# Optimization experiments

Measured on AMD Instinct MI355X. Metric: run time of the kernel, lower is better.

Reference implementation:

```python
import jax, jax.numpy as jnp
from jax import lax
import numpy as np

BS, T, DA, DZ, K = 64, 512, 16, 32, 3


def _lstm_layer(x, Wih, Whh, bih, bhh):
    # x: [B, T, in], PyTorch LSTM gate order i,f,g,o; zero initial state
    B = x.shape[0]
    H = Whh.shape[1]
    b = bih + bhh

    def step(carry, xt):
        h, c = carry
        g = xt @ Wih.T + h @ Whh.T + b  # [B, 4H]
        i, f, gg, o = jnp.split(g, 4, axis=-1)
        c = jax.nn.sigmoid(f) * c + jax.nn.sigmoid(i) * jnp.tanh(gg)
        h = jax.nn.sigmoid(o) * jnp.tanh(c)
        return (h, c), h

    h0 = jnp.zeros((B, H), x.dtype)
    _, hs = lax.scan(step, (h0, h0), jnp.swapaxes(x, 0, 1))
    return jnp.swapaxes(hs, 0, 1)


def setup_inputs() -> dict:
    key = jax.random.key(0)
    ks = jax.random.split(key, 12)
    a = jax.random.normal(ks[0], (BS, T, DA), jnp.float32)
    # mixture dynamics / emission matrices, kept near identity for stability
    A = 0.95 * jnp.eye(DZ, dtype=jnp.float32) + 0.02 * jax.random.normal(ks[1], (K, T, DZ, DZ), jnp.float32)
    C = jnp.eye(DA, DZ, dtype=jnp.float32) + 0.05 * jax.random.normal(ks[2], (K, T, DA, DZ), jnp.float32)
    R = 0.1 * jnp.eye(DA, dtype=jnp.float32)
    Q = 0.1 * jnp.eye(DZ, dtype=jnp.float32)
    mu0 = jnp.zeros((DZ,), jnp.float32)
    sigma0 = jnp.eye(DZ, dtype=jnp.float32)
    H4 = 4 * K  # LSTM hidden size = K
    Wih0 = 0.1 * jax.random.normal(ks[3], (H4, DA), jnp.float32)
    Whh0 = 0.1 * jax.random.normal(ks[4], (H4, K), jnp.float32)
    bih0 = 0.1 * jax.random.normal(ks[5], (H4,), jnp.float32)
    bhh0 = 0.1 * jax.random.normal(ks[6], (H4,), jnp.float32)
    Wih1 = 0.1 * jax.random.normal(ks[7], (H4, K), jnp.float32)
    Whh1 = 0.1 * jax.random.normal(ks[8], (H4, K), jnp.float32)
    bih1 = 0.1 * jax.random.normal(ks[9], (H4,), jnp.float32)
    bhh1 = 0.1 * jax.random.normal(ks[10], (H4,), jnp.float32)
    return {"a": a, "A": A, "C": C, "R": R, "Q": Q, "mu0": mu0, "sigma0": sigma0,
            "Wih0": Wih0, "Whh0": Whh0, "bih0": bih0, "bhh0": bhh0,
            "Wih1": Wih1, "Whh1": Whh1, "bih1": bih1, "bhh1": bhh1}


def reference(a, A, C, R, Q, mu0, sigma0, Wih0, Whh0, bih0, bhh0, Wih1, Whh1, bih1, bhh1):
    bs, T, da = a.shape
    dz = A.shape[-1]
    # dynamics network: 2-layer LSTM + softmax mixture weights alpha [bs,T,K]
    h = _lstm_layer(a, Wih0, Whh0, bih0, bhh0)
    h = _lstm_layer(h, Wih1, Whh1, bih1, bhh1)
    alpha = jax.nn.softmax(h, axis=-1)
    # mix per-mode matrices; time-major [T,bs,.,.]
    At = jnp.einsum('btk,ktij->tbij', alpha, A)
    Ct = jnp.einsum('btk,ktij->tbij', alpha, C)
    a_tm = jnp.swapaxes(a, 0, 1)  # [T,bs,da]
    I = jnp.eye(dz, dtype=a.dtype)
    mu_f0 = jnp.broadcast_to(mu0, (bs, dz))
    sig_f0 = jnp.broadcast_to(sigma0, (bs, dz, dz))

    def fstep(carry, inp):
        mu_f, mu_p, sig_p = carry  # prev filtered mean, predicted mean/cov
        a_t, A_t, C_t = inp
        # NOTE: residual uses previous *filtered* mean, matching the source code
        r = a_t - jnp.einsum('bij,bj->bi', C_t, mu_f)
        Ct_T = jnp.swapaxes(C_t, -1, -2)
        S = C_t @ sig_p @ Ct_T + R
        Kg = sig_p @ Ct_T @ jnp.linalg.inv(S)
        mu_new = mu_p + jnp.einsum('bij,bj->bi', Kg, r)
        sig_new = (I - Kg @ C_t) @ sig_p
        mu_p_new = jnp.einsum('bij,bj->bi', A_t, mu_new)
        sig_p_new = A_t @ sig_new @ jnp.swapaxes(A_t, -1, -2) + Q
        return (mu_new, mu_p_new, sig_p_new), (mu_new, sig_new, mu_p_new, sig_p_new)

    _, (mu_f, sig_f, mu_p, sig_p) = lax.scan(
        fstep, (mu_f0, mu_f0, sig_f0), (a_tm, At, Ct))

    # RTS smoothing (backward recursion), faithful to smooth()
    def sstep(carry, inp):
        mu_n, sig_n = carry
        mu_ft, sig_ft, mu_pt, sig_pt, A_next = inp
        J = sig_ft @ jnp.swapaxes(A_next, -1, -2) @ jnp.linalg.inv(sig_pt)
        mu_s = mu_ft + jnp.einsum('bij,bj->bi', J, mu_n - mu_pt)
        sig_s = sig_ft + J @ (sig_n - sig_pt)
        return (mu_s, sig_s), (mu_s, sig_s)

    _, (mu_s_rest, sig_s_rest) = lax.scan(
        sstep, (mu_f[-1], sig_f[-1]),
        (mu_f[:-1], sig_f[:-1], mu_p[:-1], sig_p[:-1], At[1:]),
        reverse=True)
    mu_s = jnp.concatenate([mu_s_rest, mu_f[-1:]], axis=0)   # [T,bs,dz]
    sig_s = jnp.concatenate([sig_s_rest, sig_f[-1:]], axis=0)  # [T,bs,dz,dz]
    out = jnp.concatenate([mu_s, sig_s.reshape(T, bs, dz * dz)], axis=-1)
    return jnp.swapaxes(out, 0, 1)  # [bs, T, dz + dz*dz]
```

## Files before the change

kernel.cpp:

```cpp
#include <hip/hip_runtime.h>
#include <hip/hip_bf16.h>

#define BSZ 64
#define TT  512
#define DA  16
#define DZ  32
#define NG  12
#define NT  256

typedef __hip_bfloat16 bf;

#define FP32_R0 0x3DCCCCCDu

__device__ __forceinline__ int mode_(const void* Rm){
  return (((const unsigned*)Rm)[0] == FP32_R0) ? 0 : 1;
}
__device__ __forceinline__ float LD(const void* p, size_t i, int b16){
  return b16 ? __bfloat162float(((const bf*)p)[i]) : ((const float*)p)[i];
}
__device__ __forceinline__ void STO(void* p, size_t i, float v, int b16){
  if (b16) ((bf*)p)[i] = __float2bfloat16(v);
  else     ((float*)p)[i] = v;
}
__device__ __forceinline__ float osan_(double vd, float code){
// ... 27 lines not shown
    for (int g=0;g<NG;++g){
      #pragma unroll
      for (int j=0;j<3;++j){ w0[g][j]=LD(Whh0,(size_t)g*3+j,b16); wi1[g][j]=LD(Wih1,(size_t)g*3+j,b16); w1[g][j]=LD(Whh1,(size_t)g*3+j,b16); }
      bb[g] = LD(bih1,g,b16) + LD(bhh1,g,b16);
    }
    float h1[3]={0,0,0}, c1[3]={0,0,0}, h2[3]={0,0,0}, c2[3]={0,0,0};
    for (int t=0;t<TT;++t){
      const float* xr = sxw + t*NG;
      float g1[NG];
      #pragma unroll
      for (int g=0;g<NG;++g) g1[g] = xr[g] + w0[g][0]*h1[0]+w0[g][1]*h1[1]+w0[g][2]*h1[2];
      #pragma unroll
      for (int j=0;j<3;++j){
        float iv=sigm_(g1[j]), fv=sigm_(g1[3+j]), gv=tanh_(g1[6+j]), ov=sigm_(g1[9+j]);
        c1[j] = fv*c1[j] + iv*gv;
        h1[j] = ov*tanh_(c1[j]);
      }
      float g2[NG];
      #pragma unroll
      for (int g=0;g<NG;++g) g2[g] = bb[g] + wi1[g][0]*h1[0]+wi1[g][1]*h1[1]+wi1[g][2]*h1[2]
                                            + w1[g][0]*h2[0]+w1[g][1]*h2[1]+w1[g][2]*h2[2];
      #pragma unroll
      for (int j=0;j<3;++j){
        float iv=sigm_(g2[j]), fv=sigm_(g2[3+j]), gv=tanh_(g2[6+j]), ov=sigm_(g2[9+j]);
        c2[j] = fv*c2[j] + iv*gv;
        h2[j] = ov*tanh_(c2[j]);
      }
      float m = fmaxf(h2[0], fmaxf(h2[1], h2[2]));
      float e0=__expf(h2[0]-m), e1=__expf(h2[1]-m), e2=__expf(h2[2]-m);
      float inv = 1.0f/(e0+e1+e2);
      salp[t*3+0]=e0*inv; salp[t*3+1]=e1*inv; salp[t*3+2]=e2*inv;
    }
  }
  __syncthreads();
}

__global__ __launch_bounds__(256) void k_alpha(
  const void* __restrict__ a, const void* __restrict__ Rm,
  const void* __restrict__ Wih0, const void* __restrict__ Whh0,
  const void* __restrict__ bih0, const void* __restrict__ bhh0,
  const void* __restrict__ Wih1, const void* __restrict__ Whh1,
  const void* __restrict__ bih1, const void* __restrict__ bhh1,
  float* __restrict__ alws)
{
  const int b16 = mode_(Rm);
  const int b = blockIdx.x, tid = threadIdx.x;
  __shared__ float sxw[TT*NG];
  __shared__ float salp[TT*3];
  alpha_stage_(b, tid, NT, b16, a, Wih0, bih0, bhh0, Whh0, Wih1, Whh1, bih1, bhh1,
               sxw, salp);
  for (int e=tid;e<TT*3;e+=NT) alws[(size_t)b*TT*3+e] = salp[e];
}

__global__ __launch_bounds__(256) void k_fwd(
  const void* __restrict__ a, const void* __restrict__ Am,
  const void* __restrict__ Cm, const void* __restrict__ Rm,
  const void* __restrict__ Qm, const void* __restrict__ mu0,
  const void* __restrict__ sig0,
  const void* __restrict__ Wih0, const void* __restrict__ Whh0,
  const void* __restrict__ bih0, const void* __restrict__ bhh0,
  const void* __restrict__ Wih1, const void* __restrict__ Whh1,
  const void* __restrict__ bih1, const void* __restrict__ bhh1,
  const float* __restrict__ alws,
  void* __restrict__ out)
{
  const int b16 = mode_(Rm);
  const int b = blockIdx.x, tid = threadIdx.x;
  __shared__ double dpool[4240];
  __shared__ float sAt[1056], sCt[528], sQ[1056], sR[272], sPCt[544], sKg[544];
  __shared__ float salp[TT*3];
  __shared__ double dMu[32], dMup[32], dr[16];
  double* dPp  = dpool;
  double* dAP  = dpool+1056;
  double* dKCP = dpool+2112;
  double* dCP  = dpool+3168;
  double* dAugS= dpool+3696;
  double* dMinv= dpool+3968;

  if (alws){
    for (int e=tid;e<TT*3;e+=NT) salp[e] = alws[(size_t)b*TT*3+e];
    __syncthreads();
  } else {
    alpha_stage_(b, tid, NT, b16, a, Wih0, bih0, bhh0, Whh0, Wih1, Whh1, bih1, bhh1,
                 (float*)dpool, salp);
  }

  for (int e=tid;e<1024;e+=NT){ int i=e>>5,j=e&31;
    sQ[i*33+j]  = LD(Qm,e,b16);
    dPp[i*33+j] = (double)LD(sig0,e,b16); }
  for (int e=tid;e<256;e+=NT){ int i=e>>4,j=e&15; sR[i*17+j] = LD(Rm,e,b16); }
  if (tid<32){ double m = (double)LD(mu0,tid,b16); dMu[tid]=m; dMup[tid]=m; }
  __syncthreads();

  const int i0 = tid>>5, j0 = tid&31;
  const int i4 = tid>>4, j4 = tid&15;

  float pA0[4],pA1[4],pA2[4],pC0[2],pC1[2],pC2[2];
  {
    size_t o0=0, o1=(size_t)TT*1024, o2=(size_t)2*TT*1024;
    #pragma unroll
    for (int q=0;q<4;++q){ int e=tid+q*NT; pA0[q]=LD(Am,o0+e,b16); pA1[q]=LD(Am,o1+e,b16); pA2[q]=LD(Am,o2+e,b16); }
    size_t c0=0, c1=(size_t)TT*512, c2=(size_t)2*TT*512;
    #pragma unroll
    for (int q=0;q<2;++q){ int e=tid+q*NT; pC0[q]=LD(Cm,c0+e,b16); pC1[q]=LD(Cm,c1+e,b16); pC2[q]=LD(Cm,c2+e,b16); }
  }

  for (int t=0;t<TT;++t){
    const size_t ob = ((size_t)b*TT+t)*1056;
    {
      float a0=salp[t*3+0], a1=salp[t*3+1], a2=salp[t*3+2];
      #pragma unroll
      for (int q=0;q<4;++q){ int e=tid+q*NT; int i=e>>5,j=e&31;
        sAt[i*33+j] = a0*pA0[q]+a1*pA1[q]+a2*pA2[q]; }
      #pragma unroll
      for (int q=0;q<2;++q){ int e=tid+q*NT; int i=e>>5,j=e&31;
        sCt[i*33+j] = a0*pC0[q]+a1*pC1[q]+a2*pC2[q]; }
    }
    if (t+1<TT){
      size_t o0=(size_t)(t+1)*1024, o1=(size_t)(TT+t+1)*1024, o2=(size_t)(2*TT+t+1)*1024;
      #pragma unroll
      for (int q=0;q<4;++q){ int e=tid+q*NT; pA0[q]=LD(Am,o0+e,b16); pA1[q]=LD(Am,o1+e,b16); pA2[q]=LD(Am,o2+e,b16); }
      size_t c0=(size_t)(t+1)*512, c1=(size_t)(TT+t+1)*512, c2=(size_t)(2*TT+t+1)*512;
      #pragma unroll
      for (int q=0;q<2;++q){ int e=tid+q*NT; pC0[q]=LD(Cm,c0+e,b16); pC1[q]=LD(Cm,c1+e,b16); pC2[q]=LD(Cm,c2+e,b16); }
    }
    __syncthreads();

    {
      double col[32];
      #pragma unroll
      for (int k=0;k<32;++k) col[k] = dPp[k*33+j0];
      double A0=0.0, A1=0.0;
      #pragma unroll
      for (int k=0;k<32;++k){
        A0 += (double)sCt[i0*33+k]*col[k];
        A1 += (double)sCt[(i0+8)*33+k]*col[k]; }
      dCP[i0*33+j0]=A0; dCP[(i0+8)*33+j0]=A1;
      double B0=0.0, B1v=0.0;
      #pragma unroll
      for (int m=0;m<32;++m){ double cv=(double)sCt[j4*33+m];
        B0  += dPp[i4*33+m]*cv;
        B1v += dPp[(i4+16)*33+m]*cv; }
      sPCt[i4*17+j4]=(float)B0; sPCt[(i4+16)*17+j4]=(float)B1v;
    }
    if (tid<16){ double s = (double)LD(a,((size_t)b*TT+t)*DA+tid,b16);
      #pragma unroll
      for (int k=0;k<32;++k) s -= (double)sCt[tid*33+k]*dMu[k];
      dr[tid]=s; }
    __syncthreads();

    if (tid < 64){
      #pragma unroll
      for (int u=0;u<4;++u){ int e=(tid<<2)+u; int i=e>>4, j=e&15;
        double v=(double)sR[i*17+j];
        #pragma unroll
        for (int k=0;k<32;++k) v += dCP[i*33+k]*(double)sCt[j*33+k];
        dAugS[i*17+j]=v; }
      const int r = tid>>2, q = tid&3, cbase = q*8;
      double Rg[8];
      #pragma unroll
      for (int u=0;u<8;++u){
        int c = cbase+u;
        Rg[u] = (c<16) ? dAugS[r*17+c] : ((c-16)==r ? 1.0 : 0.0);
      }
      #pragma unroll
      for (int kp=0;kp<16;++kp){
        double pv = __shfl(Rg[kp&7], (kp<<2)|(kp>>3), 64);
        if (!(fabs(pv)>1e-300)) pv=1.0;
        double ip = 1.0/pv;
        if (r==kp){
          #pragma unroll
          for (int u=0;u<8;++u){ int c=cbase+u; if (c>kp) Rg[u]*=ip; }
        }
        double rf = __shfl(Rg[kp&7], (tid&0x3C)|(kp>>3), 64);
        #pragma unroll
        for (int u=0;u<8;++u){
          double pr = __shfl(Rg[u], (kp<<2)|q, 64);
          int c=cbase+u;
          if (r!=kp && c>kp) Rg[u] -= rf*pr;
        }
      }
      if (q>=2){
        #pragma unroll
        for (int u=0;u<8;++u){ int k=cbase+u-16; dMinv[r*17+k]=Rg[u]; }
      }
    } else {
      for (int e=tid-64; e<1024; e+=192){ int i=e>>5,j=e&31; double acc=0.0;
        #pragma unroll
        for (int k=0;k<32;++k) acc += (double)sAt[i*33+k]*dPp[k*33+j];
        dAP[i*33+j]=acc; }
    }
    __syncthreads();

    {
      double col[16];
      #pragma unroll
      for (int l=0;l<16;++l) col[l] = dMinv[l*17+j4];
      double A0=0.0, A1=0.0;
      #pragma unroll
      for (int l=0;l<16;++l){
        A0 += (double)sPCt[i4*17+l]*col[l];
        A1 += (double)sPCt[(i4+16)*17+l]*col[l]; }
      sKg[i4*17+j4]=(float)A0; sKg[(i4+16)*17+j4]=(float)A1;
    }
    __syncthreads();

    {
      double col[16];
      #pragma unroll
      for (int l=0;l<16;++l) col[l] = dCP[l*33+j0];
      double A0=0.0,A1=0.0,A2=0.0,A3=0.0;
      #pragma unroll
      for (int l=0;l<16;++l){
        A0 += (double)sKg[i0*17+l]*col[l];
        A1 += (double)sKg[(i0+8)*17+l]*col[l];
        A2 += (double)sKg[(i0+16)*17+l]*col[l];
        A3 += (double)sKg[(i0+24)*17+l]*col[l]; }
      dKCP[i0*33+j0]=A0; dKCP[(i0+8)*33+j0]=A1;
      dKCP[(i0+16)*33+j0]=A2; dKCP[(i0+24)*33+j0]=A3;
    }
    if (tid<32){ double s=dMup[tid];
      #pragma unroll
      for (int k=0;k<16;++k) s += (double)sKg[tid*17+k]*dr[k];
      dMu[tid]=s;
      STO(out, ob+tid, osan_(s,5300.0f), b16); }
    __syncthreads();

    {
      double colK[32];
      #pragma unroll
      for (int k=0;k<32;++k) colK[k] = dKCP[k*33+j0];
      double pf0 = dPp[i0*33+j0]      - colK[0*0+ (0)];
      (void)pf0;
      double P0 = dPp[i0*33+j0]      - dKCP[i0*33+j0];
      double P1 = dPp[(i0+8)*33+j0]  - dKCP[(i0+8)*33+j0];
      double P2 = dPp[(i0+16)*33+j0] - dKCP[(i0+16)*33+j0];
      double P3 = dPp[(i0+24)*33+j0] - dKCP[(i0+24)*33+j0];
      STO(out, ob+32+((size_t)i0<<5)+j0,      osan_(P0,5300.0f), b16);
      STO(out, ob+32+((size_t)(i0+8)<<5)+j0,  osan_(P1,5300.0f), b16);
      STO(out, ob+32+((size_t)(i0+16)<<5)+j0, osan_(P2,5300.0f), b16);
      STO(out, ob+32+((size_t)(i0+24)<<5)+j0, osan_(P3,5300.0f), b16);
      double A0=dAP[i0*33+j0], A1=dAP[(i0+8)*33+j0],
             A2=dAP[(i0+16)*33+j0], A3=dAP[(i0+24)*33+j0];
      #pragma unroll
      for (int k=0;k<32;++k){
        A0 -= (double)sAt[i0*33+k]*colK[k];
        A1 -= (double)sAt[(i0+8)*33+k]*colK[k];
        A2 -= (double)sAt[(i0+16)*33+k]*colK[k];
        A3 -= (double)sAt[(i0+24)*33+k]*colK[k]; }
      dAP[i0*33+j0]=A0; dAP[(i0+8)*33+j0]=A1;
      dAP[(i0+16)*33+j0]=A2; dAP[(i0+24)*33+j0]=A3;
    }
    if (tid<32){ double s=0.0;
      #pragma unroll
      for (int k=0;k<32;++k) s += (double)sAt[tid*33+k]*dMu[k];
      dMup[tid]=s; }
    __syncthreads();

    {
      float rowA[32];
      #pragma unroll
      for (int k=0;k<32;++k) rowA[k] = sAt[j0*33+k];
      double A0=(double)sQ[i0*33+j0], A1=(double)sQ[(i0+8)*33+j0],
             A2=(double)sQ[(i0+16)*33+j0], A3=(double)sQ[(i0+24)*33+j0];
      #pragma unroll
      for (int k=0;k<32;++k){ double av=(double)rowA[k];
        A0 += dAP[i0*33+k]*av;
        A1 += dAP[(i0+8)*33+k]*av;
        A2 += dAP[(i0+16)*33+k]*av;
        A3 += dAP[(i0+24)*33+k]*av; }
      dPp[i0*33+j0]=A0; dPp[(i0+8)*33+j0]=A1;
      dPp[(i0+16)*33+j0]=A2; dPp[(i0+24)*33+j0]=A3;
    }
    __syncthreads();
  }
}

__global__ __launch_bounds__(256) void k_pre(
  const void* __restrict__ Am, const void* __restrict__ Qm,
  const void* __restrict__ Rm, const void* __restrict__ outv,
  const float* __restrict__ alws, float* __restrict__ rec, int t0)
{
  const int b16 = mode_(Rm);
  const int t = t0 + blockIdx.x;
  const int b = blockIdx.y;
  const int tid = threadIdx.x;
  __shared__ double dAug[2080];
  __shared__ double dmp[32];
  __shared__ float sAtc[1056], sAtn[1056], sSf[1056], sT[1056], sF[1056], sPp[1056], sJ[1056], sQ[1056];
  __shared__ float smu[32];

  size_t obase = (size_t)b*TT*1056;
  const float* al = alws + (size_t)b*TT*3;
  float c0=al[t*3+0],     c1=al[t*3+1],     c2=al[t*3+2];
  float n0=al[(t+1)*3+0], n1=al[(t+1)*3+1], n2=al[(t+1)*3+2];
  size_t oA0c=(size_t)t*1024, oA1c=(size_t)(TT+t)*1024, oA2c=(size_t)(2*TT+t)*1024;
  size_t oA0n=oA0c+1024, oA1n=oA1c+1024, oA2n=oA2c+1024;

  for (int e=tid;e<1024;e+=NT){ int i=e>>5,j=e&31;
    sAtc[i*33+j] = c0*LD(Am,oA0c+e,b16)+c1*LD(Am,oA1c+e,b16)+c2*LD(Am,oA2c+e,b16);
    sAtn[i*33+j] = n0*LD(Am,oA0n+e,b16)+n1*LD(Am,oA1n+e,b16)+n2*LD(Am,oA2n+e,b16);
    sSf[i*33+j]  = LD(outv, obase + (size_t)t*1056 + 32 + e, b16);
    sQ[i*33+j]   = LD(Qm,e,b16);
  }
  if (tid<32) smu[tid] = LD(outv, obase + (size_t)t*1056 + tid, b16);
  __syncthreads();

  for (int e=tid;e<1024;e+=NT){ int i=e>>5, j=e&31;
    double acc=0.0, accF=0.0;
    #pragma unroll
    for (int k=0;k<32;++k){
      acc  += (double)sAtc[i*33+k]*(double)sSf[k*33+j];
      accF += (double)sSf[i*33+k]*(double)sAtn[j*33+k];
    }
    sT[i*33+j]=(float)acc; sF[i*33+j]=(float)accF; }
  if (tid<32){ double s=0.0;
    #pragma unroll
    for (int k=0;k<32;++k) s += (double)sAtc[tid*33+k]*(double)smu[k];
    dmp[tid]=s; }
  __syncthreads();

  for (int e=tid;e<1024;e+=NT){ int i=e>>5, j=e&31;
    double acc=(double)sQ[i*33+j];
    #pragma unroll
    for (int k=0;k<32;++k) acc += (double)sT[i*33+k]*(double)sAtc[j*33+k];
    sPp[i*33+j]=(float)acc;
    dAug[i*65+j]=acc;
    dAug[i*65+32+j]=(i==j)?1.0:0.0; }
  __syncthreads();

  for (int kp=0;kp<32;++kp){
    double pv = dAug[kp*65+kp];
    if (!(fabs(pv)>1e-300)) pv=1.0;
    double ip = 1.0/pv;
    if (tid<64 && tid>kp) dAug[kp*65+tid] *= ip;
    __syncthreads();
    #pragma unroll
    for (int q=0;q<8;++q){ int e=tid+q*NT; int i=e>>6, j=e&63;
      if (i!=kp && j>kp) dAug[i*65+j] -= dAug[i*65+kp]*dAug[kp*65+j];
    }
    __syncthreads();
  }

  float* rp = rec + ((size_t)b*gridDim.x + (size_t)blockIdx.x)*2080;

  for (int e=tid;e<1024;e+=NT){ int i=e>>5, j=e&31; double acc=0.0;
    #pragma unroll
    for (int k=0;k<32;++k) acc += (double)sF[i*33+k]*dAug[k*65+32+j];
    float jv=(float)acc; sJ[i*33+j]=jv; rp[e]=jv; }
  __syncthreads();

  for (int e=tid;e<1024;e+=NT){ int i=e>>5, j=e&31;
    double acc=(double)sSf[i*33+j];
    #pragma unroll
    for (int k=0;k<32;++k) acc -= (double)sJ[i*33+k]*(double)sPp[k*33+j];
    rp[1024+e]=(float)acc; }
  if (tid<32){ double acc=(double)smu[tid];
    #pragma unroll
    for (int k=0;k<32;++k) acc -= (double)sJ[tid*33+k]*dmp[k];
    rp[2048+tid]=(float)acc; }
}

__global__ __launch_bounds__(256) void k_bwd(
  const void* __restrict__ Rm, void* __restrict__ outv,
  const float* __restrict__ rec, float* __restrict__ cont,
  int t0, int t1)
{
  const int b16 = mode_(Rm);
  const int b = blockIdx.x, tid = threadIdx.x;
  const int chlen = t1 - t0;
  __shared__ float sX[2][1056];
  __shared__ float sR[2080];
  size_t obase = (size_t)b*TT*1056;
  int cur = 0;
  const int i0 = tid>>5, j0 = tid&31;

  if (t1 == TT-1){
    for (int e=tid;e<1024;e+=NT){ int i=e>>5,j=e&31;
      sX[0][i*33+j] = LD(outv, obase+(size_t)(TT-1)*1056+32+e, b16); }
    if (tid<32) sX[0][tid*33+32] = LD(outv, obase+(size_t)(TT-1)*1056+tid, b16);
  } else {
    for (int e=tid;e<1056;e+=NT) sX[0][e] = cont[(size_t)b*1056+e];
  }
  float rg[9];
  {
    const float* rp = rec + ((size_t)b*chlen + (size_t)(chlen-1))*2080;
    #pragma unroll
    for (int q=0;q<9;++q){ int e=tid+q*NT; rg[q] = (e<2080)? rp[e] : 0.0f; }
  }
  __syncthreads();

  for (int t=t1-1; t>=t0; --t){
    #pragma unroll
    for (int q=0;q<9;++q){ int e=tid+q*NT; if (e<2080) sR[e]=rg[q]; }
    if (t>t0){
      const float* rp = rec + ((size_t)b*chlen + (size_t)(t-1-t0))*2080;
      #pragma unroll
      for (int q=0;q<9;++q){ int e=tid+q*NT; rg[q] = (e<2080)? rp[e] : 0.0f; }
    }
    __syncthreads();

    const float* Xc = sX[cur]; float* Xn = sX[cur^1];
    {
      float colX[32];
      #pragma unroll
      for (int k=0;k<32;++k) colX[k] = Xc[k*33+j0];
      double A0=(double)sR[1024+(i0<<5)+j0];
      double A1=(double)sR[1024+((i0+8)<<5)+j0];
      double A2=(double)sR[1024+((i0+16)<<5)+j0];
      double A3=(double)sR[1024+((i0+24)<<5)+j0];
      #pragma unroll
      for (int k=0;k<32;++k){ double xv=(double)colX[k];
        A0 += (double)sR[(i0<<5)+k]*xv;
        A1 += (double)sR[((i0+8)<<5)+k]*xv;
        A2 += (double)sR[((i0+16)<<5)+k]*xv;
        A3 += (double)sR[((i0+24)<<5)+k]*xv; }
      Xn[i0*33+j0]=(float)A0;      Xn[(i0+8)*33+j0]=(float)A1;
      Xn[(i0+16)*33+j0]=(float)A2; Xn[(i0+24)*33+j0]=(float)A3;
      size_t tb = obase+(size_t)t*1056+32;
      STO(outv, tb+((size_t)i0<<5)+j0,      osan_(A0,5700.0f), b16);
      STO(outv, tb+((size_t)(i0+8)<<5)+j0,  osan_(A1,5700.0f), b16);
      STO(outv, tb+((size_t)(i0+16)<<5)+j0, osan_(A2,5700.0f), b16);
      STO(outv, tb+((size_t)(i0+24)<<5)+j0, osan_(A3,5700.0f), b16);
    }
    if (tid<32){
      double acc=(double)sR[2048+tid];
      #pragma unroll
      for (int k=0;k<32;++k) acc += (double)sR[(tid<<5)+k]*(double)Xc[k*33+32];
      Xn[tid*33+32]=(float)acc;
      STO(outv, obase+(size_t)t*1056+tid, osan_(acc,5700.0f), b16);
    }
    __syncthreads();
    cur ^= 1;
  }
  for (int e=tid;e<1056;e+=NT) cont[(size_t)b*1056+e] = sX[cur][e];
}

__global__ __launch_bounds__(256) void k_smooth(
  const void* __restrict__ a, const void* __restrict__ Am,
  const void* __restrict__ Rm, const void* __restrict__ Qm,
  const void* __restrict__ Wih0, const void* __restrict__ Whh0,
  const void* __restrict__ bih0, const void* __restrict__ bhh0,
  const void* __restrict__ Wih1, const void* __restrict__ Whh1,
  const void* __restrict__ bih1, const void* __restrict__ bhh1,
  void* __restrict__ out)
{
  const int b16 = mode_(Rm);
  const int b = blockIdx.x, tid = threadIdx.x;
  __shared__ double dAug[2080];
  __shared__ float fp2[9504];
  __shared__ float salp[TT*3];
  __shared__ double dMun[32], dmp[32], sdm[32];
  float* sAtn = fp2;
  float* sAtc = fp2+1056;
  float* sSf  = fp2+2112;
  float* sSn  = fp2+3168;
  float* sT   = fp2+4224;
  float* sQ   = fp2+5280;
  float* sF   = fp2+6336;
  float* sPp32= fp2+7392;
  float* sJ   = fp2+8448;

  alpha_stage_(b, tid, NT, b16, a, Wih0, bih0, bhh0, Whh0, Wih1, Whh1, bih1, bhh1,
               fp2, salp);

  size_t obase = (size_t)b*TT*1056;
  for (int e=tid;e<1024;e+=NT){ int i=e>>5,j=e&31;
    sQ[i*33+j]  = LD(Qm,e,b16);
    sSn[i*33+j] = LD(out, obase + (size_t)(TT-1)*1056 + 32 + e, b16); }
  if (tid<32) dMun[tid] = (double)LD(out, obase + (size_t)(TT-1)*1056 + tid, b16);
  __syncthreads();

  for (int t=TT-2; t>=0; --t){
    float n0=salp[(t+1)*3+0], n1=salp[(t+1)*3+1], n2=salp[(t+1)*3+2];
    float c0=salp[t*3+0],     c1=salp[t*3+1],     c2=salp[t*3+2];
    size_t oA0n=(size_t)(t+1)*1024, oA1n=(size_t)(TT+t+1)*1024, oA2n=(size_t)(2*TT+t+1)*1024;
    size_t oA0c=(size_t)t*1024,     oA1c=(size_t)(TT+t)*1024,   oA2c=(size_t)(2*TT+t)*1024;
    for (int e=tid;e<1024;e+=NT){ int i=e>>5,j=e&31;
      sAtn[i*33+j] = n0*LD(Am,oA0n+e,b16)+n1*LD(Am,oA1n+e,b16)+n2*LD(Am,oA2n+e,b16);
      sAtc[i*33+j] = c0*LD(Am,oA0c+e,b16)+c1*LD(Am,oA1c+e,b16)+c2*LD(Am,oA2c+e,b16);
      sSf[i*33+j]  = LD(out, obase + (size_t)t*1056 + 32 + e, b16); }
    __syncthreads();

    for (int e=tid;e<1024;e+=NT){ int i=e>>5, j=e&31;
      double acc=0.0, accF=0.0;
      #pragma unroll
      for (int k=0;k<32;++k){
        acc  += (double)sAtc[i*33+k]*(double)sSf[k*33+j];
// ... 47 lines not shown
        #pragma unroll
        for (int k=0;k<32;++k) acc += (double)sJ[i*33+k]*((double)sSn[k*33+j]-(double)sPp32[k*33+j]);
        double res = (double)sSf[i*33+j] + acc;
        STO(out, obase+(size_t)t*1056+32+(i<<5)+j, osan_(res,5700.0f), b16);
        resv[s]=(float)res;
      }
    }
    __syncthreads();
    { int i0 = tid>>5, j = tid&31;
      for (int s=0;s<4;++s){ int i=i0+(s<<3); sSn[i*33+j]=resv[s]; } }
    __syncthreads();
  }
}

__global__ __launch_bounds__(256) void k_fill(float* o, int n, float v){
  int i = blockIdx.x*256 + threadIdx.x;
  if (i<n) o[i]=v;
}

extern "C" void kernel_launch(void* const* d_in, const int* in_sizes, int n_in,
                              void* d_out, int out_size, void* d_ws, size_t ws_size,
                              hipStream_t stream)
{
  static const int EXP[15] = {524288,1572864,786432,256,1024,32,1024,192,36,12,12,36,36,12,12};
  int ok = (n_in==15) && (out_size==34603008);
  if (ok) for (int i=0;i<15;++i) if (in_sizes[i]!=EXP[i]) ok=0;
  if (!ok){
    k_fill<<<dim3((out_size+255)/256), dim3(256), 0, stream>>>((float*)d_out, out_size, 777.0f);
    return;
  }
  const void* a=d_in[0]; const void* Am=d_in[1]; const void* Cm=d_in[2];
  const void* Rm=d_in[3]; const void* Qm=d_in[4]; const void* mu0=d_in[5];
  const void* sig0=d_in[6];
  const void* Wih0=d_in[7]; const void* Whh0=d_in[8]; const void* bih0=d_in[9];
  const void* bhh0=d_in[10]; const void* Wih1=d_in[11]; const void* Whh1=d_in[12];
  const void* bih1=d_in[13]; const void* bhh1=d_in[14];

  const long long FIXED_F = 98304LL + 67584LL;
  long long availB = (long long)ws_size;
  int CH = 0;
  if (d_ws && availB > FIXED_F*4){
    long long ch = (availB - FIXED_F*4) / (64LL*2080LL*4LL);
    CH = (int)((ch > 511) ? 511 : ch);
  }

  if (CH >= 4){
    float* wsf  = (float*)d_ws;
    float* alws = wsf;
    float* cont = wsf + 98304;
    float* rec  = wsf + 165888;

    k_alpha<<<dim3(BSZ), dim3(NT), 0, stream>>>(a, Rm,
        Wih0, Whh0, bih0, bhh0, Wih1, Whh1, bih1, bhh1, alws);
    k_fwd  <<<dim3(BSZ), dim3(NT), 0, stream>>>(a, Am, Cm, Rm, Qm, mu0, sig0,
        Wih0, Whh0, bih0, bhh0, Wih1, Whh1, bih1, bhh1, alws, d_out);

    int t1 = TT-1;
    while (t1 > 0){
      int t0 = t1 - CH; if (t0 < 0) t0 = 0;
      int len = t1 - t0;
      k_pre<<<dim3(len, BSZ), dim3(NT), 0, stream>>>(Am, Qm, Rm, d_out, alws, rec, t0);
      k_bwd<<<dim3(BSZ), dim3(NT), 0, stream>>>(Rm, d_out, rec, cont, t0, t1);
      t1 = t0;
    }
  } else {
    k_fwd   <<<dim3(BSZ), dim3(NT), 0, stream>>>(a, Am, Cm, Rm, Qm, mu0, sig0,
               Wih0, Whh0, bih0, bhh0, Wih1, Whh1, bih1, bhh1, (const float*)nullptr, d_out);
    k_smooth<<<dim3(BSZ), dim3(NT), 0, stream>>>(a, Am, Rm, Qm,
               Wih0, Whh0, bih0, bhh0, Wih1, Whh1, bih1, bhh1, d_out);
  }
}
```

Baseline: 10.92 ms.

## Run Kalman forward and backward kernels as single wavefront with register-tiled matmuls

k_fwd and k_bwd shrink from 256 to 64 threads per block. Each thread now computes 4x4 or 2x2 output tiles using float4/double2 vectorized LDS loads, with row strides padded to 34/36 for alignment. The forward covariance update is reordered to form P_f explicitly and then compute A·P_f·Aᵀ+Q, dropping the AP/KCP side-path. The aim is cheaper barriers and better register reuse in the latency-bound sequential recurrence, at the cost of each thread doing more serial FP64 work and higher register pressure.

```diff
diff --git a/kernel.cpp b/kernel.cpp
--- a/kernel.cpp
+++ b/kernel.cpp
@@ -103,7 +103,9 @@
   for (int e=tid;e<TT*3;e+=NT) alws[(size_t)b*TT*3+e] = salp[e];
 }
 
-__global__ __launch_bounds__(256) void k_fwd(
+#define F4A(f) {(f).x,(f).y,(f).z,(f).w}
+
+__global__ __launch_bounds__(64) void k_fwd(
   const void* __restrict__ a, const void* __restrict__ Am,
   const void* __restrict__ Cm, const void* __restrict__ Rm,
   const void* __restrict__ Qm, const void* __restrict__ mu0,
@@ -117,43 +119,48 @@
 {
   const int b16 = mode_(Rm);
   const int b = blockIdx.x, tid = threadIdx.x;
-  __shared__ double dpool[4240];
-  __shared__ float sAt[1056], sCt[528], sQ[1056], sR[272], sPCt[544], sKg[544];
-  __shared__ float salp[TT*3];
+  __shared__ __align__(16) double dpool[4368];
+  double* dPp  = dpool;
+  double* dPf  = dpool+1088;
+  double* dKT  = dpool+2176;
+  double* dCP  = dpool+3264;
+  double* dAugS= dpool+3808;
+  double* dMinv= dpool+4080;
+  __shared__ __align__(16) float sAt[1152];
+  __shared__ __align__(16) float sCt[576];
+  __shared__ __align__(16) float sQ[1152];
+  __shared__ __align__(16) float sKg[512];
+  __shared__ __align__(16) float sPCt[512];
+  __shared__ float sR[272], salp[TT*3];
   __shared__ double dMu[32], dMup[32], dr[16];
-  double* dPp  = dpool;
-  double* dAP  = dpool+1056;
-  double* dKCP = dpool+2112;
-  double* dCP  = dpool+3168;
-  double* dAugS= dpool+3696;
-  double* dMinv= dpool+3968;
 
   if (alws){
-    for (int e=tid;e<TT*3;e+=NT) salp[e] = alws[(size_t)b*TT*3+e];
-    __syncthreads();
+    for (int e=tid;e<TT*3;e+=64) salp[e] = alws[(size_t)b*TT*3+e];
   } else {
-    alpha_stage_(b, tid, NT, b16, a, Wih0, bih0, bhh0, Whh0, Wih1, Whh1, bih1, bhh1,
+    alpha_stage_(b, tid, 64, b16, a, Wih0, bih0, bhh0, Whh0, Wih1, Whh1, bih1, bhh1,
                  (float*)dpool, salp);
   }
 
-  for (int e=tid;e<1024;e+=NT){ int i=e>>5,j=e&31;
-    sQ[i*33+j]  = LD(Qm,e,b16);
-    dPp[i*33+j] = (double)LD(sig0,e,b16); }
-  for (int e=tid;e<256;e+=NT){ int i=e>>4,j=e&15; sR[i*17+j] = LD(Rm,e,b16); }
+  for (int e=tid;e<1024;e+=64){ int i=e>>5,j=e&31;
+    sQ[i*36+j]  = LD(Qm,e,b16);
+    dPp[i*34+j] = (double)LD(sig0,e,b16); }
+  for (int e=tid;e<256;e+=64){ int i=e>>4,j=e&15; sR[i*17+j] = LD(Rm,e,b16); }
   if (tid<32){ double m = (double)LD(mu0,tid,b16); dMu[tid]=m; dMup[tid]=m; }
   __syncthreads();
 
-  const int i0 = tid>>5, j0 = tid&31;
-  const int i4 = tid>>4, j4 = tid&15;
-
-  float pA0[4],pA1[4],pA2[4],pC0[2],pC1[2],pC2[2];
+  const int u = tid>>3, v = tid&7;
+  const int I0 = u<<2, J0 = v<<2;
+  const int i2 = u<<1, j2 = v<<1;
+
+  float pA0[16],pA1[16],pA2[16],pC0[8],pC1[8],pC2[8],pa;
   {
     size_t o0=0, o1=(size_t)TT*1024, o2=(size_t)2*TT*1024;
     #pragma unroll
-    for (int q=0;q<4;++q){ int e=tid+q*NT; pA0[q]=LD(Am,o0+e,b16); pA1[q]=LD(Am,o1+e,b16); pA2[q]=LD(Am,o2+e,b16); }
+    for (int q=0;q<16;++q){ int e=tid+(q<<6); pA0[q]=LD(Am,o0+e,b16); pA1[q]=LD(Am,o1+e,b16); pA2[q]=LD(Am,o2+e,b16); }
     size_t c0=0, c1=(size_t)TT*512, c2=(size_t)2*TT*512;
     #pragma unroll
-    for (int q=0;q<2;++q){ int e=tid+q*NT; pC0[q]=LD(Cm,c0+e,b16); pC1[q]=LD(Cm,c1+e,b16); pC2[q]=LD(Cm,c2+e,b16); }
+    for (int q=0;q<8;++q){ int e=tid+(q<<6); pC0[q]=LD(Cm,c0+e,b16); pC1[q]=LD(Cm,c1+e,b16); pC2[q]=LD(Cm,c2+e,b16); }
+    pa = (tid<16)? LD(a,((size_t)b*TT+0)*DA+tid,b16) : 0.0f;
   }
 
   for (int t=0;t<TT;++t){
@@ -161,58 +168,107 @@
     {
       float a0=salp[t*3+0], a1=salp[t*3+1], a2=salp[t*3+2];
       #pragma unroll
-      for (int q=0;q<4;++q){ int e=tid+q*NT; int i=e>>5,j=e&31;
-        sAt[i*33+j] = a0*pA0[q]+a1*pA1[q]+a2*pA2[q]; }
-      #pragma unroll
-      for (int q=0;q<2;++q){ int e=tid+q*NT; int i=e>>5,j=e&31;
-        sCt[i*33+j] = a0*pC0[q]+a1*pC1[q]+a2*pC2[q]; }
-    }
+      for (int q=0;q<16;++q){ int e=tid+(q<<6); int i=e>>5,j=e&31;
+        sAt[i*36+j] = a0*pA0[q]+a1*pA1[q]+a2*pA2[q]; }
+      #pragma unroll
+      for (int q=0;q<8;++q){ int e=tid+(q<<6); int i=e>>5,j=e&31;
+        sCt[i*36+j] = a0*pC0[q]+a1*pC1[q]+a2*pC2[q]; }
+    }
+    float cura = pa;
     if (t+1<TT){
       size_t o0=(size_t)(t+1)*1024, o1=(size_t)(TT+t+1)*1024, o2=(size_t)(2*TT+t+1)*1024;
       #pragma unroll
-      for (int q=0;q<4;++q){ int e=tid+q*NT; pA0[q]=LD(Am,o0+e,b16); pA1[q]=LD(Am,o1+e,b16); pA2[q]=LD(Am,o2+e,b16); }
+      for (int q=0;q<16;++q){ int e=tid+(q<<6); pA0[q]=LD(Am,o0+e,b16); pA1[q]=LD(Am,o1+e,b16); pA2[q]=LD(Am,o2+e,b16); }
       size_t c0=(size_t)(t+1)*512, c1=(size_t)(TT+t+1)*512, c2=(size_t)(2*TT+t+1)*512;
       #pragma unroll
-      for (int q=0;q<2;++q){ int e=tid+q*NT; pC0[q]=LD(Cm,c0+e,b16); pC1[q]=LD(Cm,c1+e,b16); pC2[q]=LD(Cm,c2+e,b16); }
-    }
-    __syncthreads();
-
-    {
-      double col[32];
-      #pragma unroll
-      for (int k=0;k<32;++k) col[k] = dPp[k*33+j0];
-      double A0=0.0, A1=0.0;
-      #pragma unroll
-      for (int k=0;k<32;++k){
-        A0 += (double)sCt[i0*33+k]*col[k];
-        A1 += (double)sCt[(i0+8)*33+k]*col[k]; }
-      dCP[i0*33+j0]=A0; dCP[(i0+8)*33+j0]=A1;
-      double B0=0.0, B1v=0.0;
-      #pragma unroll
-      for (int m=0;m<32;++m){ double cv=(double)sCt[j4*33+m];
-        B0  += dPp[i4*33+m]*cv;
-        B1v += dPp[(i4+16)*33+m]*cv; }
-      sPCt[i4*17+j4]=(float)B0; sPCt[(i4+16)*17+j4]=(float)B1v;
-    }
-    if (tid<16){ double s = (double)LD(a,((size_t)b*TT+t)*DA+tid,b16);
-      #pragma unroll
-      for (int k=0;k<32;++k) s -= (double)sCt[tid*33+k]*dMu[k];
+      for (int q=0;q<8;++q){ int e=tid+(q<<6); pC0[q]=LD(Cm,c0+e,b16); pC1[q]=LD(Cm,c1+e,b16); pC2[q]=LD(Cm,c2+e,b16); }
+      pa = (tid<16)? LD(a,((size_t)b*TT+t+1)*DA+tid,b16) : 0.0f;
+    }
+    __syncthreads();
+
+    {
+      double acc0[4]={0,0,0,0}, acc1[4]={0,0,0,0};
+      #pragma unroll
+      for (int kk=0;kk<8;++kk){
+        float4 f0 = *(const float4*)&sCt[(i2+0)*36+(kk<<2)];
+        float4 f1 = *(const float4*)&sCt[(i2+1)*36+(kk<<2)];
+        float a0v[4]=F4A(f0), a1v[4]=F4A(f1);
+        #pragma unroll
+        for (int s=0;s<4;++s){
+          int k=(kk<<2)+s;
+          double2 b0 = *(const double2*)&dPp[k*34+J0];
+          double2 b1 = *(const double2*)&dPp[k*34+J0+2];
+          double av0=(double)a0v[s], av1=(double)a1v[s];
+          acc0[0]+=av0*b0.x; acc0[1]+=av0*b0.y; acc0[2]+=av0*b1.x; acc0[3]+=av0*b1.y;
+          acc1[0]+=av1*b0.x; acc1[1]+=av1*b0.y; acc1[2]+=av1*b1.x; acc1[3]+=av1*b1.y;
+        }
+      }
+      *(double2*)&dCP[(i2+0)*34+J0]   = make_double2(acc0[0],acc0[1]);
+      *(double2*)&dCP[(i2+0)*34+J0+2] = make_double2(acc0[2],acc0[3]);
+      *(double2*)&dCP[(i2+1)*34+J0]   = make_double2(acc1[0],acc1[1]);
+      *(double2*)&dCP[(i2+1)*34+J0+2] = make_double2(acc1[2],acc1[3]);
+    }
+    {
+      double acc[4][2]={{0,0},{0,0},{0,0},{0,0}};
+      #pragma unroll
+      for (int s=0;s<4;++s){
+        #pragma unroll
+        for (int kk=0;kk<8;++kk){
+          double2 p0=*(const double2*)&dPp[(I0+s)*34+(kk<<2)];
+          double2 p1=*(const double2*)&dPp[(I0+s)*34+(kk<<2)+2];
+          double pr[4]={p0.x,p0.y,p1.x,p1.y};
+          float4 c0v=*(const float4*)&sCt[(j2+0)*36+(kk<<2)];
+          float4 c1v=*(const float4*)&sCt[(j2+1)*36+(kk<<2)];
+          float c0r[4]=F4A(c0v), c1r[4]=F4A(c1v);
+          #pragma unroll
+          for (int s2=0;s2<4;++s2){
+            acc[s][0]+=pr[s2]*(double)c0r[s2];
+            acc[s][1]+=pr[s2]*(double)c1r[s2]; }
+        }
+      }
+      #pragma unroll
+      for (int s=0;s<4;++s){
+        sPCt[(I0+s)*16+(j2+0)]=(float)acc[s][0];
+        sPCt[(I0+s)*16+(j2+1)]=(float)acc[s][1]; }
+    }
+    if (tid<16){ double s=(double)cura;
+      #pragma unroll
+      for (int k=0;k<32;++k) s -= (double)sCt[tid*36+k]*dMu[k];
       dr[tid]=s; }
     __syncthreads();
 
-    if (tid < 64){
-      #pragma unroll
-      for (int u=0;u<4;++u){ int e=(tid<<2)+u; int i=e>>4, j=e&15;
-        double v=(double)sR[i*17+j];
-        #pragma unroll
-        for (int k=0;k<32;++k) v += dCP[i*33+k]*(double)sCt[j*33+k];
-        dAugS[i*17+j]=v; }
+    {
+      double acc[2][2];
+      acc[0][0]=(double)sR[(i2+0)*17+(j2+0)]; acc[0][1]=(double)sR[(i2+0)*17+(j2+1)];
+      acc[1][0]=(double)sR[(i2+1)*17+(j2+0)]; acc[1][1]=(double)sR[(i2+1)*17+(j2+1)];
+      #pragma unroll
+      for (int kk=0;kk<8;++kk){
+        double2 A0a=*(const double2*)&dCP[(i2+0)*34+(kk<<2)];
+        double2 A0b=*(const double2*)&dCP[(i2+0)*34+(kk<<2)+2];
+        double2 A1a=*(const double2*)&dCP[(i2+1)*34+(kk<<2)];
+        double2 A1b=*(const double2*)&dCP[(i2+1)*34+(kk<<2)+2];
+        float4 B0=*(const float4*)&sCt[(j2+0)*36+(kk<<2)];
+        float4 B1=*(const float4*)&sCt[(j2+1)*36+(kk<<2)];
+        double a0r[4]={A0a.x,A0a.y,A0b.x,A0b.y}, a1r[4]={A1a.x,A1a.y,A1b.x,A1b.y};
+        float b0r[4]=F4A(B0), b1r[4]=F4A(B1);
+        #pragma unroll
+        for (int s=0;s<4;++s){
+          acc[0][0]+=a0r[s]*(double)b0r[s]; acc[0][1]+=a0r[s]*(double)b1r[s];
+          acc[1][0]+=a1r[s]*(double)b0r[s]; acc[1][1]+=a1r[s]*(double)b1r[s];
+        }
+      }
+      dAugS[(i2+0)*17+(j2+0)]=acc[0][0]; dAugS[(i2+0)*17+(j2+1)]=acc[0][1];
+      dAugS[(i2+1)*17+(j2+0)]=acc[1][0]; dAugS[(i2+1)*17+(j2+1)]=acc[1][1];
+    }
+    __syncthreads();
+
+    {
       const int r = tid>>2, q = tid&3, cbase = q*8;
       double Rg[8];
       #pragma unroll
-      for (int u=0;u<8;++u){
-        int c = cbase+u;
-        Rg[u] = (c<16) ? dAugS[r*17+c] : ((c-16)==r ? 1.0 : 0.0);
+      for (int uu=0;uu<8;++uu){
+        int c = cbase+uu;
+        Rg[uu] = (c<16) ? dAugS[r*17+c] : ((c-16)==r ? 1.0 : 0.0);
       }
       #pragma unroll
       for (int kp=0;kp<16;++kp){
@@ -221,107 +277,153 @@
         double ip = 1.0/pv;
         if (r==kp){
           #pragma unroll
-          for (int u=0;u<8;++u){ int c=cbase+u; if (c>kp) Rg[u]*=ip; }
+          for (int uu=0;uu<8;++uu){ int c=cbase+uu; if (c>kp) Rg[uu]*=ip; }
         }
         double rf = __shfl(Rg[kp&7], (tid&0x3C)|(kp>>3), 64);
         #pragma unroll
-        for (int u=0;u<8;++u){
-          double pr = __shfl(Rg[u], (kp<<2)|q, 64);
-          int c=cbase+u;
-          if (r!=kp && c>kp) Rg[u] -= rf*pr;
+        for (int uu=0;uu<8;++uu){
+          double pr = __shfl(Rg[uu], (kp<<2)|q, 64);
+          int c=cbase+uu;
+          if (r!=kp && c>kp) Rg[uu] -= rf*pr;
         }
       }
       if (q>=2){
         #pragma unroll
-        for (int u=0;u<8;++u){ int k=cbase+u-16; dMinv[r*17+k]=Rg[u]; }
-      }
-    } else {
-      for (int e=tid-64; e<1024; e+=192){ int i=e>>5,j=e&31; double acc=0.0;
-        #pragma unroll
-        for (int k=0;k<32;++k) acc += (double)sAt[i*33+k]*dPp[k*33+j];
-        dAP[i*33+j]=acc; }
-    }
-    __syncthreads();
-
-    {
-      double col[16];
-      #pragma unroll
-      for (int l=0;l<16;++l) col[l] = dMinv[l*17+j4];
-      double A0=0.0, A1=0.0;
+        for (int uu=0;uu<8;++uu){ int k=cbase+uu-16; dMinv[r*18+k]=Rg[uu]; }
+      }
+    }
+    __syncthreads();
+
+    {
+      double acc[4][2]={{0,0},{0,0},{0,0},{0,0}};
       #pragma unroll
       for (int l=0;l<16;++l){
-        A0 += (double)sPCt[i4*17+l]*col[l];
-        A1 += (double)sPCt[(i4+16)*17+l]*col[l]; }
-      sKg[i4*17+j4]=(float)A0; sKg[(i4+16)*17+j4]=(float)A1;
-    }
-    __syncthreads();
-
-    {
-      double col[16];
-      #pragma unroll
-      for (int l=0;l<16;++l) col[l] = dCP[l*33+j0];
-      double A0=0.0,A1=0.0,A2=0.0,A3=0.0;
-      #pragma unroll
-      for (int l=0;l<16;++l){
-        A0 += (double)sKg[i0*17+l]*col[l];
-        A1 += (double)sKg[(i0+8)*17+l]*col[l];
-        A2 += (double)sKg[(i0+16)*17+l]*col[l];
-        A3 += (double)sKg[(i0+24)*17+l]*col[l]; }
-      dKCP[i0*33+j0]=A0; dKCP[(i0+8)*33+j0]=A1;
-      dKCP[(i0+16)*33+j0]=A2; dKCP[(i0+24)*33+j0]=A3;
+        double2 m0=*(const double2*)&dMinv[l*18+j2];
+        #pragma unroll
+        for (int s=0;s<4;++s){
+          double pv=(double)sPCt[(I0+s)*16+l];
+          acc[s][0]+=pv*m0.x; acc[s][1]+=pv*m0.y; }
+      }
+      #pragma unroll
+      for (int s=0;s<4;++s){
+        sKg[(I0+s)*16+(j2+0)]=(float)acc[s][0];
+        sKg[(I0+s)*16+(j2+1)]=(float)acc[s][1]; }
+    }
+    __syncthreads();
+
+    {
+      double acc[4][4]={};
+      #pragma unroll
+      for (int ll=0;ll<4;++ll){
+        float4 g0=*(const float4*)&sKg[(I0+0)*16+(ll<<2)];
+        float4 g1=*(const float4*)&sKg[(I0+1)*16+(ll<<2)];
+        float4 g2=*(const float4*)&sKg[(I0+2)*16+(ll<<2)];
+        float4 g3=*(const float4*)&sKg[(I0+3)*16+(ll<<2)];
+        float gr[4][4]={F4A(g0),F4A(g1),F4A(g2),F4A(g3)};
+        #pragma unroll
+        for (int s2=0;s2<4;++s2){
+          int l=(ll<<2)+s2;
+          double2 b0=*(const double2*)&dCP[l*34+J0];
+          double2 b1=*(const double2*)&dCP[l*34+J0+2];
+          double bb0=b0.x, bb1=b0.y, bb2=b1.x, bb3=b1.y;
+          #pragma unroll
+          for (int s=0;s<4;++s){
+            double gv=(double)gr[s][s2];
+            acc[s][0]+=gv*bb0; acc[s][1]+=gv*bb1; acc[s][2]+=gv*bb2; acc[s][3]+=gv*bb3; }
+        }
+      }
+      #pragma unroll
+      for (int s=0;s<4;++s){
+        *(double2*)&dKT[(I0+s)*34+J0]   = make_double2(acc[s][0],acc[s][1]);
+        *(double2*)&dKT[(I0+s)*34+J0+2] = make_double2(acc[s][2],acc[s][3]); }
     }
     if (tid<32){ double s=dMup[tid];
       #pragma unroll
-      for (int k=0;k<16;++k) s += (double)sKg[tid*17+k]*dr[k];
+      for (int k=0;k<16;++k) s += (double)sKg[tid*16+k]*dr[k];
       dMu[tid]=s;
       STO(out, ob+tid, osan_(s,5300.0f), b16); }
     __syncthreads();
 
-    {
-      double colK[32];
-      #pragma unroll
-      for (int k=0;k<32;++k) colK[k] = dKCP[k*33+j0];
-      double pf0 = dPp[i0*33+j0]      - colK[0*0+ (0)];
-      (void)pf0;
-      double P0 = dPp[i0*33+j0]      - dKCP[i0*33+j0];
-      double P1 = dPp[(i0+8)*33+j0]  - dKCP[(i0+8)*33+j0];
-      double P2 = dPp[(i0+16)*33+j0] - dKCP[(i0+16)*33+j0];
-      double P3 = dPp[(i0+24)*33+j0] - dKCP[(i0+24)*33+j0];
-      STO(out, ob+32+((size_t)i0<<5)+j0,      osan_(P0,5300.0f), b16);
-      STO(out, ob+32+((size_t)(i0+8)<<5)+j0,  osan_(P1,5300.0f), b16);
-      STO(out, ob+32+((size_t)(i0+16)<<5)+j0, osan_(P2,5300.0f), b16);
-      STO(out, ob+32+((size_t)(i0+24)<<5)+j0, osan_(P3,5300.0f), b16);
-      double A0=dAP[i0*33+j0], A1=dAP[(i0+8)*33+j0],
-             A2=dAP[(i0+16)*33+j0], A3=dAP[(i0+24)*33+j0];
-      #pragma unroll
-      for (int k=0;k<32;++k){
-        A0 -= (double)sAt[i0*33+k]*colK[k];
-        A1 -= (double)sAt[(i0+8)*33+k]*colK[k];
-        A2 -= (double)sAt[(i0+16)*33+k]*colK[k];
-        A3 -= (double)sAt[(i0+24)*33+k]*colK[k]; }
-      dAP[i0*33+j0]=A0; dAP[(i0+8)*33+j0]=A1;
-      dAP[(i0+16)*33+j0]=A2; dAP[(i0+24)*33+j0]=A3;
+    #pragma unroll
+    for (int s=0;s<4;++s){
+      double2 p0=*(const double2*)&dPp[(I0+s)*34+J0];
+      double2 p1=*(const double2*)&dPp[(I0+s)*34+J0+2];
+      double2 k0=*(const double2*)&dKT[(I0+s)*34+J0];
+      double2 k1=*(const double2*)&dKT[(I0+s)*34+J0+2];
+      double f0=p0.x-k0.x, f1=p0.y-k0.y, f2=p1.x-k1.x, f3=p1.y-k1.y;
+      *(double2*)&dPf[(I0+s)*34+J0]   = make_double2(f0,f1);
+      *(double2*)&dPf[(I0+s)*34+J0+2] = make_double2(f2,f3);
+      size_t rb = ob+32+((size_t)(I0+s)<<5)+J0;
+      STO(out,rb+0,osan_(f0,5300.0f),b16); STO(out,rb+1,osan_(f1,5300.0f),b16);
+      STO(out,rb+2,osan_(f2,5300.0f),b16); STO(out,rb+3,osan_(f3,5300.0f),b16);
+    }
+    __syncthreads();
+
+    {
+      double acc[4][4]={};
+      #pragma unroll
+      for (int kk=0;kk<8;++kk){
+        float4 fA0=*(const float4*)&sAt[(I0+0)*36+(kk<<2)];
+        float4 fA1=*(const float4*)&sAt[(I0+1)*36+(kk<<2)];
+        float4 fA2=*(const float4*)&sAt[(I0+2)*36+(kk<<2)];
+        float4 fA3=*(const float4*)&sAt[(I0+3)*36+(kk<<2)];
+        float ar[4][4]={F4A(fA0),F4A(fA1),F4A(fA2),F4A(fA3)};
+        #pragma unroll
+        for (int s2=0;s2<4;++s2){
+          int k=(kk<<2)+s2;
+          double2 b0=*(const double2*)&dPf[k*34+J0];
+          double2 b1=*(const double2*)&dPf[k*34+J0+2];
+          double bb0=b0.x, bb1=b0.y, bb2=b1.x, bb3=b1.y;
+          #pragma unroll
+          for (int s=0;s<4;++s){
+            double av=(double)ar[s][s2];
+            acc[s][0]+=av*bb0; acc[s][1]+=av*bb1; acc[s][2]+=av*bb2; acc[s][3]+=av*bb3; }
+        }
+      }
+      #pragma unroll
+      for (int s=0;s<4;++s){
+        *(double2*)&dKT[(I0+s)*34+J0]   = make_double2(acc[s][0],acc[s][1]);
+        *(double2*)&dKT[(I0+s)*34+J0+2] = make_double2(acc[s][2],acc[s][3]); }
     }
     if (tid<32){ double s=0.0;
       #pragma unroll
-      for (int k=0;k<32;++k) s += (double)sAt[tid*33+k]*dMu[k];
+      for (int k=0;k<32;++k) s += (double)sAt[tid*36+k]*dMu[k];
       dMup[tid]=s; }
     __syncthreads();
 
     {
-      float rowA[32];
-      #pragma unroll
-      for (int k=0;k<32;++k) rowA[k] = sAt[j0*33+k];
-      double A0=(double)sQ[i0*33+j0], A1=(double)sQ[(i0+8)*33+j0],
-             A2=(double)sQ[(i0+16)*33+j0], A3=(double)sQ[(i0+24)*33+j0];
-      #pragma unroll
-      for (int k=0;k<32;++k){ double av=(double)rowA[k];
-        A0 += dAP[i0*33+k]*av;
-        A1 += dAP[(i0+8)*33+k]*av;
-        A2 += dAP[(i0+16)*33+k]*av;
-        A3 += dAP[(i0+24)*33+k]*av; }
-      dPp[i0*33+j0]=A0; dPp[(i0+8)*33+j0]=A1;
-      dPp[(i0+16)*33+j0]=A2; dPp[(i0+24)*33+j0]=A3;
+      double acc[4][4];
+      #pragma unroll
+      for (int s=0;s<4;++s){
+        float4 qv=*(const float4*)&sQ[(I0+s)*36+J0];
+        acc[s][0]=(double)qv.x; acc[s][1]=(double)qv.y; acc[s][2]=(double)qv.z; acc[s][3]=(double)qv.w; }
+      #pragma unroll
+      for (int kk=0;kk<8;++kk){
+        double tr[4][4];
+        #pragma unroll
+        for (int s=0;s<4;++s){
+          double2 t0=*(const double2*)&dKT[(I0+s)*34+(kk<<2)];
+          double2 t1=*(const double2*)&dKT[(I0+s)*34+(kk<<2)+2];
+          tr[s][0]=t0.x; tr[s][1]=t0.y; tr[s][2]=t1.x; tr[s][3]=t1.y; }
+        float4 fB0=*(const float4*)&sAt[(J0+0)*36+(kk<<2)];
+        float4 fB1=*(const float4*)&sAt[(J0+1)*36+(kk<<2)];
+        float4 fB2=*(const float4*)&sAt[(J0+2)*36+(kk<<2)];
+        float4 fB3=*(const float4*)&sAt[(J0+3)*36+(kk<<2)];
+        float br[4][4]={F4A(fB0),F4A(fB1),F4A(fB2),F4A(fB3)};
+        #pragma unroll
+        for (int s2=0;s2<4;++s2){
+          #pragma unroll
+          for (int s=0;s<4;++s){
+            acc[s][0]+=tr[s][s2]*(double)br[0][s2];
+            acc[s][1]+=tr[s][s2]*(double)br[1][s2];
+            acc[s][2]+=tr[s][s2]*(double)br[2][s2];
+            acc[s][3]+=tr[s][s2]*(double)br[3][s2]; }
+        }
+      }
+      #pragma unroll
+      for (int s=0;s<4;++s){
+        *(double2*)&dPp[(I0+s)*34+J0]   = make_double2(acc[s][0],acc[s][1]);
+        *(double2*)&dPp[(I0+s)*34+J0+2] = make_double2(acc[s][2],acc[s][3]); }
     }
     __syncthreads();
   }
@@ -412,7 +514,7 @@
     rp[2048+tid]=(float)acc; }
 }
 
-__global__ __launch_bounds__(256) void k_bwd(
+__global__ __launch_bounds__(64) void k_bwd(
   const void* __restrict__ Rm, void* __restrict__ outv,
   const float* __restrict__ rec, float* __restrict__ cont,
   int t0, int t1)
@@ -420,71 +522,88 @@
   const int b16 = mode_(Rm);
   const int b = blockIdx.x, tid = threadIdx.x;
   const int chlen = t1 - t0;
-  __shared__ float sX[2][1056];
-  __shared__ float sR[2080];
+  __shared__ __align__(16) float sX[2][1152];
+  __shared__ __align__(16) float sR[2080];
   size_t obase = (size_t)b*TT*1056;
   int cur = 0;
-  const int i0 = tid>>5, j0 = tid&31;
+  const int u = tid>>3, v = tid&7, I0 = u<<2, J0 = v<<2;
 
   if (t1 == TT-1){
-    for (int e=tid;e<1024;e+=NT){ int i=e>>5,j=e&31;
-      sX[0][i*33+j] = LD(outv, obase+(size_t)(TT-1)*1056+32+e, b16); }
-    if (tid<32) sX[0][tid*33+32] = LD(outv, obase+(size_t)(TT-1)*1056+tid, b16);
+    for (int e=tid;e<1024;e+=64){ int i=e>>5,j=e&31;
+      sX[0][i*36+j] = LD(outv, obase+(size_t)(TT-1)*1056+32+e, b16); }
+    if (tid<32) sX[0][tid*36+32] = LD(outv, obase+(size_t)(TT-1)*1056+tid, b16);
   } else {
-    for (int e=tid;e<1056;e+=NT) sX[0][e] = cont[(size_t)b*1056+e];
-  }
-  float rg[9];
+    for (int e=tid;e<1056;e+=64){ int k=e/33, j=e-33*k;
+      sX[0][k*36+j] = cont[(size_t)b*1056+e]; }
+  }
+  float rg[33];
   {
     const float* rp = rec + ((size_t)b*chlen + (size_t)(chlen-1))*2080;
     #pragma unroll
-    for (int q=0;q<9;++q){ int e=tid+q*NT; rg[q] = (e<2080)? rp[e] : 0.0f; }
+    for (int q=0;q<33;++q){ int e=tid+(q<<6); rg[q] = (e<2080)? rp[e] : 0.0f; }
   }
   __syncthreads();
 
   for (int t=t1-1; t>=t0; --t){
     #pragma unroll
-    for (int q=0;q<9;++q){ int e=tid+q*NT; if (e<2080) sR[e]=rg[q]; }
+    for (int q=0;q<33;++q){ int e=tid+(q<<6); if (e<2080) sR[e]=rg[q]; }
     if (t>t0){
       const float* rp = rec + ((size_t)b*chlen + (size_t)(t-1-t0))*2080;
       #pragma unroll
-      for (int q=0;q<9;++q){ int e=tid+q*NT; rg[q] = (e<2080)? rp[e] : 0.0f; }
+      for (int q=0;q<33;++q){ int e=tid+(q<<6); rg[q] = (e<2080)? rp[e] : 0.0f; }
     }
     __syncthreads();
 
     const float* Xc = sX[cur]; float* Xn = sX[cur^1];
     {
-      float colX[32];
-      #pragma unroll
-      for (int k=0;k<32;++k) colX[k] = Xc[k*33+j0];
-      double A0=(double)sR[1024+(i0<<5)+j0];
-      double A1=(double)sR[1024+((i0+8)<<5)+j0];
-      double A2=(double)sR[1024+((i0+16)<<5)+j0];
-      double A3=(double)sR[1024+((i0+24)<<5)+j0];
-      #pragma unroll
-      for (int k=0;k<32;++k){ double xv=(double)colX[k];
-        A0 += (double)sR[(i0<<5)+k]*xv;
-        A1 += (double)sR[((i0+8)<<5)+k]*xv;
-        A2 += (double)sR[((i0+16)<<5)+k]*xv;
-        A3 += (double)sR[((i0+24)<<5)+k]*xv; }
-      Xn[i0*33+j0]=(float)A0;      Xn[(i0+8)*33+j0]=(float)A1;
-      Xn[(i0+16)*33+j0]=(float)A2; Xn[(i0+24)*33+j0]=(float)A3;
+      double acc[4][4];
+      #pragma unroll
+      for (int s=0;s<4;++s){
+        float4 bq=*(const float4*)&sR[1024+((I0+s)<<5)+J0];
+        acc[s][0]=(double)bq.x; acc[s][1]=(double)bq.y; acc[s][2]=(double)bq.z; acc[s][3]=(double)bq.w; }
+      #pragma unroll
+      for (int kk=0;kk<8;++kk){
+        float4 j0=*(const float4*)&sR[((I0+0)<<5)+(kk<<2)];
+        float4 j1=*(const float4*)&sR[((I0+1)<<5)+(kk<<2)];
+        float4 j2v=*(const float4*)&sR[((I0+2)<<5)+(kk<<2)];
+        float4 j3=*(const float4*)&sR[((I0+3)<<5)+(kk<<2)];
+        float jr[4][4]={F4A(j0),F4A(j1),F4A(j2v),F4A(j3)};
+        float4 x0=*(const float4*)&Xc[((kk<<2)+0)*36+J0];
+        float4 x1=*(const float4*)&Xc[((kk<<2)+1)*36+J0];
+        float4 x2=*(const float4*)&Xc[((kk<<2)+2)*36+J0];
+        float4 x3=*(const float4*)&Xc[((kk<<2)+3)*36+J0];
+        float xr[4][4]={F4A(x0),F4A(x1),F4A(x2),F4A(x3)};
+        #pragma unroll
+        for (int s2=0;s2<4;++s2){
+          #pragma unroll
+          for (int s=0;s<4;++s){
+            double jv=(double)jr[s][s2];
+            acc[s][0]+=jv*(double)xr[s2][0]; acc[s][1]+=jv*(double)xr[s2][1];
+            acc[s][2]+=jv*(double)xr[s2][2]; acc[s][3]+=jv*(double)xr[s2][3]; }
+        }
+      }
       size_t tb = obase+(size_t)t*1056+32;
-      STO(outv, tb+((size_t)i0<<5)+j0,      osan_(A0,5700.0f), b16);
-      STO(outv, tb+((size_t)(i0+8)<<5)+j0,  osan_(A1,5700.0f), b16);
-      STO(outv, tb+((size_t)(i0+16)<<5)+j0, osan_(A2,5700.0f), b16);
-      STO(outv, tb+((size_t)(i0+24)<<5)+j0, osan_(A3,5700.0f), b16);
+      #pragma unroll
+      for (int s=0;s<4;++s){
+        #pragma unroll
+        for (int c=0;c<4;++c){
+          Xn[(I0+s)*36+J0+c]=(float)acc[s][c];
+          STO(outv, tb+(((size_t)(I0+s))<<5)+J0+c, osan_(acc[s][c],5700.0f), b16); }
+      }
     }
     if (tid<32){
-      double acc=(double)sR[2048+tid];
-      #pragma unroll
-      for (int k=0;k<32;++k) acc += (double)sR[(tid<<5)+k]*(double)Xc[k*33+32];
-      Xn[tid*33+32]=(float)acc;
-      STO(outv, obase+(size_t)t*1056+tid, osan_(acc,5700.0f), b16);
+      double accm=(double)sR[2048+tid];
+      #pragma unroll
+      for (int k=0;k<32;++k) accm += (double)sR[(tid<<5)+k]*(double)Xc[k*36+32];
+      Xn[tid*36+32]=(float)accm;
+      STO(outv, obase+(size_t)t*1056+tid, osan_(accm,5700.0f), b16);
     }
     __syncthreads();
     cur ^= 1;
   }
-  for (int e=tid;e<1056;e+=NT) cont[(size_t)b*1056+e] = sX[cur][e];
+  { const float* Xf = sX[cur];
+    for (int e=tid;e<1056;e+=64){ int k=e/33, j=e-33*k;
+      cont[(size_t)b*1056+e] = Xf[k*36+j]; } }
 }
 
 __global__ __launch_bounds__(256) void k_smooth(
@@ -638,7 +757,7 @@
 
     k_alpha<<<dim3(BSZ), dim3(NT), 0, stream>>>(a, Rm,
         Wih0, Whh0, bih0, bhh0, Wih1, Whh1, bih1, bhh1, alws);
-    k_fwd  <<<dim3(BSZ), dim3(NT), 0, stream>>>(a, Am, Cm, Rm, Qm, mu0, sig0,
+    k_fwd  <<<dim3(BSZ), dim3(64), 0, stream>>>(a, Am, Cm, Rm, Qm, mu0, sig0,
         Wih0, Whh0, bih0, bhh0, Wih1, Whh1, bih1, bhh1, alws, d_out);
 
     int t1 = TT-1;
@@ -646,11 +765,11 @@
       int t0 = t1 - CH; if (t0 < 0) t0 = 0;
       int len = t1 - t0;
       k_pre<<<dim3(len, BSZ), dim3(NT), 0, stream>>>(Am, Qm, Rm, d_out, alws, rec, t0);
-      k_bwd<<<dim3(BSZ), dim3(NT), 0, stream>>>(Rm, d_out, rec, cont, t0, t1);
+      k_bwd<<<dim3(BSZ), dim3(64), 0, stream>>>(Rm, d_out, rec, cont, t0, t1);
       t1 = t0;
     }
   } else {
-    k_fwd   <<<dim3(BSZ), dim3(NT), 0, stream>>>(a, Am, Cm, Rm, Qm, mu0, sig0,
+    k_fwd   <<<dim3(BSZ), dim3(64), 0, stream>>>(a, Am, Cm, Rm, Qm, mu0, sig0,
                Wih0, Whh0, bih0, bhh0, Wih1, Whh1, bih1, bhh1, (const float*)nullptr, d_out);
     k_smooth<<<dim3(BSZ), dim3(NT), 0, stream>>>(a, Am, Rm, Qm,
                Wih0, Whh0, bih0, bhh0, Wih1, Whh1, bih1, bhh1, d_out);
```

New measurement: 15.61 ms. +42.9%, slower.
